# Performance work log

Hardware: AMD Instinct MI355X
Metric: run time of the kernel (lower is better)

Reference implementation:

```python
import jax, jax.numpy as jnp
import numpy as np

L = 512          # angles_max_length
R_CA = 3.8       # C-alpha - C-alpha virtual bond length (AB model)


def _B_mat(a, b):
    # Rigid transform of the AB C-alpha model: rot(alpha) about z, rot(beta), translate R along x.
    ca, sa = jnp.cos(a), jnp.sin(a)
    cb, sb = jnp.cos(b), jnp.sin(b)
    z = jnp.zeros_like(a)
    o = jnp.ones_like(a)
    rows = [
        [ca, -sa * cb,  sa * sb, R_CA * ca],
        [sa,  ca * cb, -ca * sb, R_CA * sa],
        [z,   sb,       cb,      z],
        [z,   z,        z,       o],
    ]
    return jnp.stack([jnp.stack(r, -1) for r in rows], -2)  # (..., 4, 4)


def _dB_da(a, b):
    ca, sa = jnp.cos(a), jnp.sin(a)
    cb, sb = jnp.cos(b), jnp.sin(b)
    z = jnp.zeros_like(a)
    rows = [
        [-sa, -ca * cb,  ca * sb, -R_CA * sa],
        [ ca, -sa * cb,  sa * sb,  R_CA * ca],
        [z, z, z, z],
        [z, z, z, z],
    ]
    return jnp.stack([jnp.stack(r, -1) for r in rows], -2)


def _dB_db(a, b):
    ca, sa = jnp.cos(a), jnp.sin(a)
    cb, sb = jnp.cos(b), jnp.sin(b)
    z = jnp.zeros_like(a)
    rows = [
        [z,  sa * sb,  sa * cb, z],
        [z, -ca * sb, -ca * cb, z],
        [z,  cb,      -sb,      z],
        [z, z, z, z],
    ]
    return jnp.stack([jnp.stack(r, -1) for r in rows], -2)


def setup_inputs() -> dict:
    key = jax.random.key(0)
    k1, k2, k3 = jax.random.split(key, 3)
    input_angles = jax.random.normal(k1, (32, 2, L), dtype=jnp.float32)
    input_coords = jax.random.normal(k2, (32, 3 * (L + 1)), dtype=jnp.float32)
    angles_length = jax.random.randint(k3, (32,), 0, L, dtype=jnp.int32)
    return {"input_angles": input_angles, "input_coords": input_coords,
            "angles_length": angles_length}


def reference(input_angles, input_coords, angles_length):
    Bsz = input_angles.shape[0]
    alpha = input_angles[:, 0, :]  # (B, L)
    beta = input_angles[:, 1, :]

    Bm = _B_mat(alpha, beta)  # (B, L, 4, 4)
    # Prefix products M_i = B_0 @ ... @ B_i (order-preserving associative scan).
    M = jax.lax.associative_scan(lambda x, y: x @ y, Bm, axis=1)
    eye = jnp.broadcast_to(jnp.eye(4, dtype=Bm.dtype), (Bsz, 1, 4, 4))
    M_prev = jnp.concatenate([eye, M[:, :-1]], axis=1)  # M_{i-1}

    # Rigid-transform inverse of M_i: [R^T, -R^T t; 0 1]
    Rm = M[..., :3, :3]
    t = M[..., :3, 3:]
    Rt = jnp.swapaxes(Rm, -1, -2)
    bottom = jnp.broadcast_to(jnp.array([0., 0., 0., 1.], Bm.dtype), (Bsz, L, 1, 4))
    Minv = jnp.concatenate(
        [jnp.concatenate([Rt, -(Rt @ t)], axis=-1), bottom], axis=-2)

    # F_i^q = M_{i-1} dB_i/dq M_i^{-1};  dr_j/dq_i = F_i^q r_j^h  (for j > i)
    Fa = M_prev @ _dB_da(alpha, beta) @ Minv  # (B, L, 4, 4)
    Fb = M_prev @ _dB_db(alpha, beta) @ Minv

    coords = input_coords.reshape(Bsz, L + 1, 3)
    rh = jnp.concatenate([coords, jnp.ones((Bsz, L + 1, 1), coords.dtype)], -1)

    ga = jnp.einsum('blij,bmj->blmi', Fa, rh)[..., :3]  # (B, L, L+1, 3)
    gb = jnp.einsum('blij,bmj->blmi', Fb, rh)[..., :3]

    i = jnp.arange(L)[:, None]
    j = jnp.arange(L + 1)[None, :]
    lens = angles_length[:, None, None]
    mask = ((j > i) & (i < lens) & (j <= lens))[..., None]
    ga = jnp.where(mask, ga, 0.0)
    gb = jnp.where(mask, gb, 0.0)

    out = jnp.stack([ga, gb], axis=1)  # (B, 2, L, L+1, 3)
    return out.reshape(Bsz, 2, 3 * L * (L + 1))
```

## Files before the change

### kernel.cpp

```cpp
#include <hip/hip_runtime.h>

#define LSEQ 512
#define RCA 3.8f

struct Aff { float m[3][4]; };

__device__ __forceinline__ Aff compose(const Aff& A, const Aff& B) {
    Aff C;
#pragma unroll
    for (int i = 0; i < 3; ++i) {
#pragma unroll
        for (int j = 0; j < 4; ++j) {
            float v = A.m[i][0] * B.m[0][j] + A.m[i][1] * B.m[1][j] + A.m[i][2] * B.m[2][j];
            if (j == 3) v += A.m[i][3];
            C.m[i][j] = v;
        }
    }
    return C;
}

__device__ __forceinline__ Aff shflUp(const Aff& a, int d) {
    Aff r;
#pragma unroll
    for (int i = 0; i < 3; ++i)
#pragma unroll
        for (int j = 0; j < 4; ++j)
            r.m[i][j] = __shfl_up(a.m[i][j], d, 64);
    return r;
}

__device__ __forceinline__ Aff makeB(float ca, float sa, float cb, float sb) {
    Aff B;
    B.m[0][0] = ca;  B.m[0][1] = -sa * cb; B.m[0][2] =  sa * sb; B.m[0][3] = RCA * ca;
    B.m[1][0] = sa;  B.m[1][1] =  ca * cb; B.m[1][2] = -ca * sb; B.m[1][3] = RCA * sa;
    B.m[2][0] = 0.f; B.m[2][1] =  sb;      B.m[2][2] =  cb;      B.m[2][3] = 0.f;
    return B;
}

__global__ __launch_bounds__(512) void scan_kernel(const float* __restrict__ angles,
                                                   float* __restrict__ F) {
    const int b = blockIdx.x;
    const int tid = threadIdx.x;
    const int lane = tid & 63;
    const int w = tid >> 6;

    __shared__ float sT[8][12];

    const float a  = angles[(size_t)b * 1024 + tid];
    const float be = angles[(size_t)b * 1024 + 512 + tid];
    float sa, ca, sb, cb;
    __sincosf(a, &sa, &ca);
    __sincosf(be, &sb, &cb);

    Aff S = makeB(ca, sa, cb, sb);
#pragma unroll
    for (int d = 1; d < 64; d <<= 1) {
        Aff o = shflUp(S, d);
        if (lane >= d) S = compose(o, S);
    }

    if (lane == 63) {
#pragma unroll
        for (int k = 0; k < 12; ++k) sT[w][k] = S.m[k / 4][k % 4];
    }
    __syncthreads();

    Aff E;
#pragma unroll
    for (int i = 0; i < 3; ++i)
#pragma unroll
        for (int j = 0; j < 4; ++j) E.m[i][j] = (i == j) ? 1.f : 0.f;
    for (int k = 0; k < w; ++k) {
        Aff T;
#pragma unroll
        for (int q = 0; q < 12; ++q) T.m[q / 4][q % 4] = sT[k][q];
        E = compose(E, T);
    }

    const Aff Sp = shflUp(S, 1);
    const Aff M = compose(E, S);
    Aff Mprev;
    if (lane == 0) Mprev = E;
    else           Mprev = compose(E, Sp);

    float Rt[3][3], ti[3];
#pragma unroll
    for (int i = 0; i < 3; ++i)
#pragma unroll
        for (int j = 0; j < 3; ++j) Rt[i][j] = M.m[j][i];
#pragma unroll
    for (int i = 0; i < 3; ++i)
        ti[i] = -(M.m[0][i] * M.m[0][3] + M.m[1][i] * M.m[1][3] + M.m[2][i] * M.m[2][3]);

    float d0[4] = {-sa, -ca * cb,  ca * sb, -RCA * sa};
    float d1[4] = { ca, -sa * cb,  sa * sb,  RCA * ca};
    float e01 =  sa * sb, e02 =  sa * cb;
    float e11 = -ca * sb, e12 = -ca * cb;
    float e21 =  cb,      e22 = -sb;

    float Ga[3][4], Gb[3][4];
#pragma unroll
    for (int i = 0; i < 3; ++i) {
        float p0 = Mprev.m[i][0], p1 = Mprev.m[i][1], p2 = Mprev.m[i][2];
#pragma unroll
        for (int j = 0; j < 4; ++j) Ga[i][j] = p0 * d0[j] + p1 * d1[j];
        Gb[i][0] = 0.f;
        Gb[i][1] = p0 * e01 + p1 * e11 + p2 * e21;
        Gb[i][2] = p0 * e02 + p1 * e12 + p2 * e22;
        Gb[i][3] = 0.f;
    }

    float W[24];
#pragma unroll
    for (int i = 0; i < 3; ++i) {
#pragma unroll
        for (int j = 0; j < 3; ++j) {
            W[i * 4 + j]      = Ga[i][0] * Rt[0][j] + Ga[i][1] * Rt[1][j] + Ga[i][2] * Rt[2][j];
            W[12 + i * 4 + j] = Gb[i][0] * Rt[0][j] + Gb[i][1] * Rt[1][j] + Gb[i][2] * Rt[2][j];
        }
        W[i * 4 + 3]      = Ga[i][0] * ti[0] + Ga[i][1] * ti[1] + Ga[i][2] * ti[2] + Ga[i][3];
        W[12 + i * 4 + 3] = Gb[i][0] * ti[0] + Gb[i][1] * ti[1] + Gb[i][2] * ti[2] + Gb[i][3];
    }

    float4* w4 = reinterpret_cast<float4*>(F + ((size_t)b * LSEQ + tid) * 24);
    const float4* s4 = reinterpret_cast<const float4*>(W);
#pragma unroll
    for (int q = 0; q < 6; ++q) w4[q] = s4[q];
}

__device__ __forceinline__ void st3_nt(float* p, float x, float y, float z) {
    __builtin_nontemporal_store(x, p);
    __builtin_nontemporal_store(y, p + 1);
    __builtin_nontemporal_store(z, p + 2);
}

__global__ __launch_bounds__(256) void emit_kernel(const float* __restrict__ F,
                                                   const float* __restrict__ coords,
                                                   const int* __restrict__ lens,
                                                   float* __restrict__ out) {
    const int b = blockIdx.y;
    const int l0 = blockIdx.x * 8;
    const int tid = threadIdx.x;

    __shared__ float sF[192];
    if (tid < 192) sF[tid] = F[((size_t)b * LSEQ + l0) * 24 + tid];
    __syncthreads();

    const int len = lens[b];
    const float* cp = coords + (size_t)b * 1539;

    const int m0 = tid, m1 = tid + 256, m2 = tid + 512;
    const float cx0 = cp[m0 * 3], cy0 = cp[m0 * 3 + 1], cz0 = cp[m0 * 3 + 2];
    const float cx1 = cp[m1 * 3], cy1 = cp[m1 * 3 + 1], cz1 = cp[m1 * 3 + 2];
    const bool has2 = (m2 < 513);
    float cx2 = 0.f, cy2 = 0.f, cz2 = 0.f;
    if (has2) { cx2 = cp[m2 * 3]; cy2 = cp[m2 * 3 + 1]; cz2 = cp[m2 * 3 + 2]; }

#pragma unroll
    for (int i = 0; i < 8; ++i) {
        const int l = l0 + i;
        const float* f = sF + i * 24;
        const float f00 = f[0],  f01 = f[1],  f02 = f[2],  f03 = f[3];
        const float f10 = f[4],  f11 = f[5],  f12 = f[6],  f13 = f[7];
        const float f20 = f[8],  f21 = f[9],  f22 = f[10], f23 = f[11];
        const float g00 = f[12], g01 = f[13], g02 = f[14], g03 = f[15];
        const float g10 = f[16], g11 = f[17], g12 = f[18], g13 = f[19];
        const float g20 = f[20], g21 = f[21], g22 = f[22], g23 = f[23];

        const size_t baseA = ((size_t)(b * 2) * LSEQ + l) * 1539;
        const size_t baseB = baseA + (size_t)LSEQ * 1539;
        const bool rowActive = (l < len);

        auto emit1 = [&](int m, float x, float y, float z) {
            const float s = (rowActive && (m > l) && (m <= len)) ? 1.f : 0.f;
            st3_nt(out + baseA + (size_t)m * 3,
                   s * (f00 * x + f01 * y + f02 * z + f03),
                   s * (f10 * x + f11 * y + f12 * z + f13),
                   s * (f20 * x + f21 * y + f22 * z + f23));
            st3_nt(out + baseB + (size_t)m * 3,
                   s * (g00 * x + g01 * y + g02 * z + g03),
                   s * (g10 * x + g11 * y + g12 * z + g13),
                   s * (g20 * x + g21 * y + g22 * z + g23));
        };

        emit1(m0, cx0, cy0, cz0);
        emit1(m1, cx1, cy1, cz1);
        if (has2) emit1(m2, cx2, cy2, cz2);
    }
}

extern "C" void kernel_launch(void* const* d_in, const int* in_sizes, int n_in,
                              void* d_out, int out_size, void* d_ws, size_t ws_size,
                              hipStream_t stream) {
    const float* angles = (const float*)d_in[0];
    const float* coords = (const float*)d_in[1];
    const int*   lens   = (const int*)d_in[2];
    float* out = (float*)d_out;
    float* F = (float*)d_ws;

    scan_kernel<<<32, 512, 0, stream>>>(angles, F);
    emit_kernel<<<dim3(64, 32), 256, 0, stream>>>(F, coords, lens, out);
}
```

Before: 235.6 us.

## Flatten emit kernel so each thread writes one contiguous float4 of output

Replaces the row-tiled emit kernel, which issued scalar strided nontemporal stores, with a flat kernel in which each thread computes four consecutive output floats and writes them as one aligned float4. Output indices are decoded into channel, angle, atom and component with integer divides, and coordinates and F rows are read straight from global memory and cache. This aims to fully coalesce the large output write stream, at the cost of extra index arithmetic, redundant F and coordinate loads, and dropping the nontemporal hint.

```diff
diff --git a/kernel.cpp b/kernel.cpp
--- a/kernel.cpp
+++ b/kernel.cpp
@@ -128,65 +128,46 @@
     for (int q = 0; q < 6; ++q) w4[q] = s4[q];
 }
 
-__device__ __forceinline__ void st3_nt(float* p, float x, float y, float z) {
-    __builtin_nontemporal_store(x, p);
-    __builtin_nontemporal_store(y, p + 1);
-    __builtin_nontemporal_store(z, p + 2);
-}
+__global__ __launch_bounds__(256) void emit_flat(const float* __restrict__ F,
+                                                 const float* __restrict__ coords,
+                                                 const int* __restrict__ lens,
+                                                 float* __restrict__ out) {
+    const int b = blockIdx.y;
+    const unsigned o = (blockIdx.x * 256u + threadIdx.x) * 4u;
 
-__global__ __launch_bounds__(256) void emit_kernel(const float* __restrict__ F,
-                                                   const float* __restrict__ coords,
-                                                   const int* __restrict__ lens,
-                                                   float* __restrict__ out) {
-    const int b = blockIdx.y;
-    const int l0 = blockIdx.x * 8;
-    const int tid = threadIdx.x;
+    const unsigned len = (unsigned)lens[b];
+    const float* __restrict__ Cb = coords + (size_t)b * 1539;
+    const float* __restrict__ Fb = F + (size_t)b * LSEQ * 24;
 
-    __shared__ float sF[192];
-    if (tid < 192) sF[tid] = F[((size_t)b * LSEQ + l0) * 24 + tid];
-    __syncthreads();
+    unsigned ch = (o >= 787968u) ? 1u : 0u;
+    unsigned r2 = o - ch * 787968u;
+    unsigned l  = r2 / 1539u;
+    unsigned r3 = r2 - l * 1539u;
+    unsigned m  = r3 / 3u;
+    unsigned c  = r3 - m * 3u;
 
-    const int len = lens[b];
-    const float* cp = coords + (size_t)b * 1539;
+    float v[4];
+#pragma unroll
+    for (int k = 0; k < 4; ++k) {
+        const float4 f = *reinterpret_cast<const float4*>(Fb + (l * 24u + ch * 12u + c * 4u));
+        const float x = Cb[m * 3u];
+        const float y = Cb[m * 3u + 1u];
+        const float z = Cb[m * 3u + 2u];
+        const bool act = (m > l) & (l < len) & (m <= len);
+        const float s = act ? 1.f : 0.f;
+        v[k] = s * (f.x * x + f.y * y + f.z * z + f.w);
 
-    const int m0 = tid, m1 = tid + 256, m2 = tid + 512;
-    const float cx0 = cp[m0 * 3], cy0 = cp[m0 * 3 + 1], cz0 = cp[m0 * 3 + 2];
-    const float cx1 = cp[m1 * 3], cy1 = cp[m1 * 3 + 1], cz1 = cp[m1 * 3 + 2];
-    const bool has2 = (m2 < 513);
-    float cx2 = 0.f, cy2 = 0.f, cz2 = 0.f;
-    if (has2) { cx2 = cp[m2 * 3]; cy2 = cp[m2 * 3 + 1]; cz2 = cp[m2 * 3 + 2]; }
+        if (++c == 3u) {
+            c = 0u;
+            if (++m == 513u) {
+                m = 0u;
+                if (++l == 512u) { l = 0u; ++ch; }
+            }
+        }
+    }
 
-#pragma unroll
-    for (int i = 0; i < 8; ++i) {
-        const int l = l0 + i;
-        const float* f = sF + i * 24;
-        const float f00 = f[0],  f01 = f[1],  f02 = f[2],  f03 = f[3];
-        const float f10 = f[4],  f11 = f[5],  f12 = f[6],  f13 = f[7];
-        const float f20 = f[8],  f21 = f[9],  f22 = f[10], f23 = f[11];
-        const float g00 = f[12], g01 = f[13], g02 = f[14], g03 = f[15];
-        const float g10 = f[16], g11 = f[17], g12 = f[18], g13 = f[19];
-        const float g20 = f[20], g21 = f[21], g22 = f[22], g23 = f[23];
-
-        const size_t baseA = ((size_t)(b * 2) * LSEQ + l) * 1539;
-        const size_t baseB = baseA + (size_t)LSEQ * 1539;
-        const bool rowActive = (l < len);
-
-        auto emit1 = [&](int m, float x, float y, float z) {
-            const float s = (rowActive && (m > l) && (m <= len)) ? 1.f : 0.f;
-            st3_nt(out + baseA + (size_t)m * 3,
-                   s * (f00 * x + f01 * y + f02 * z + f03),
-                   s * (f10 * x + f11 * y + f12 * z + f13),
-                   s * (f20 * x + f21 * y + f22 * z + f23));
-            st3_nt(out + baseB + (size_t)m * 3,
-                   s * (g00 * x + g01 * y + g02 * z + g03),
-                   s * (g10 * x + g11 * y + g12 * z + g13),
-                   s * (g20 * x + g21 * y + g22 * z + g23));
-        };
-
-        emit1(m0, cx0, cy0, cz0);
-        emit1(m1, cx1, cy1, cz1);
-        if (has2) emit1(m2, cx2, cy2, cz2);
-    }
+    float4 r; r.x = v[0]; r.y = v[1]; r.z = v[2]; r.w = v[3];
+    *reinterpret_cast<float4*>(out + (size_t)b * 1575936u + o) = r;
 }
 
 extern "C" void kernel_launch(void* const* d_in, const int* in_sizes, int n_in,
@@ -199,5 +180,5 @@
     float* F = (float*)d_ws;
 
     scan_kernel<<<32, 512, 0, stream>>>(angles, F);
-    emit_kernel<<<dim3(64, 32), 256, 0, stream>>>(F, coords, lens, out);
+    emit_flat<<<dim3(1539, 32), 256, 0, stream>>>(F, coords, lens, out);
 }
```

Measured after the change: 302.6 us. +28.5%, slower.

## Stage emit rows in LDS and write them out as aligned float4 stores

Applied to the files above, without the earlier changes.

The emit kernel now writes each output row's computed triples into shared-memory buffers, padded so the global row start lands on a 16-byte boundary. The row is then written to global memory with coalesced float4 stores, plus scalar head and tail stores, in place of strided 3-float nontemporal scalar stores. This targets write-coalescing inefficiency on the output, which is about 100 MB. It adds two barriers per row, serialises the row loop (unroll 1), and drops the nontemporal hint.

```diff
diff --git a/kernel.cpp b/kernel.cpp
--- a/kernel.cpp
+++ b/kernel.cpp
@@ -126,12 +126,6 @@
     const float4* s4 = reinterpret_cast<const float4*>(W);
 #pragma unroll
     for (int q = 0; q < 6; ++q) w4[q] = s4[q];
-}
-
-__device__ __forceinline__ void st3_nt(float* p, float x, float y, float z) {
-    __builtin_nontemporal_store(x, p);
-    __builtin_nontemporal_store(y, p + 1);
-    __builtin_nontemporal_store(z, p + 2);
 }
 
 __global__ __launch_bounds__(256) void emit_kernel(const float* __restrict__ F,
@@ -143,8 +137,10 @@
     const int tid = threadIdx.x;
 
     __shared__ float sF[192];
+    __shared__ float sA[1544];
+    __shared__ float sB[1544];
+
     if (tid < 192) sF[tid] = F[((size_t)b * LSEQ + l0) * 24 + tid];
-    __syncthreads();
 
     const int len = lens[b];
     const float* cp = coords + (size_t)b * 1539;
@@ -156,7 +152,9 @@
     float cx2 = 0.f, cy2 = 0.f, cz2 = 0.f;
     if (has2) { cx2 = cp[m2 * 3]; cy2 = cp[m2 * 3 + 1]; cz2 = cp[m2 * 3 + 2]; }
 
-#pragma unroll
+    __syncthreads();
+
+#pragma unroll 1
     for (int i = 0; i < 8; ++i) {
         const int l = l0 + i;
         const float* f = sF + i * 24;
@@ -167,25 +165,48 @@
         const float g10 = f[16], g11 = f[17], g12 = f[18], g13 = f[19];
         const float g20 = f[20], g21 = f[21], g22 = f[22], g23 = f[23];
 
-        const size_t baseA = ((size_t)(b * 2) * LSEQ + l) * 1539;
-        const size_t baseB = baseA + (size_t)LSEQ * 1539;
         const bool rowActive = (l < len);
-
-        auto emit1 = [&](int m, float x, float y, float z) {
+        const unsigned phase = (3u * (unsigned)l) & 3u;
+        const unsigned head  = (4u - phase) & 3u;
+        const unsigned pad   = phase;
+
+        auto cw = [&](int m, float x, float y, float z) {
             const float s = (rowActive && (m > l) && (m <= len)) ? 1.f : 0.f;
-            st3_nt(out + baseA + (size_t)m * 3,
-                   s * (f00 * x + f01 * y + f02 * z + f03),
-                   s * (f10 * x + f11 * y + f12 * z + f13),
-                   s * (f20 * x + f21 * y + f22 * z + f23));
-            st3_nt(out + baseB + (size_t)m * 3,
-                   s * (g00 * x + g01 * y + g02 * z + g03),
-                   s * (g10 * x + g11 * y + g12 * z + g13),
-                   s * (g20 * x + g21 * y + g22 * z + g23));
+            const int base = pad + m * 3;
+            sA[base + 0] = s * (f00 * x + f01 * y + f02 * z + f03);
+            sA[base + 1] = s * (f10 * x + f11 * y + f12 * z + f13);
+            sA[base + 2] = s * (f20 * x + f21 * y + f22 * z + f23);
+            sB[base + 0] = s * (g00 * x + g01 * y + g02 * z + g03);
+            sB[base + 1] = s * (g10 * x + g11 * y + g12 * z + g13);
+            sB[base + 2] = s * (g20 * x + g21 * y + g22 * z + g23);
         };
-
-        emit1(m0, cx0, cy0, cz0);
-        emit1(m1, cx1, cy1, cz1);
-        if (has2) emit1(m2, cx2, cy2, cz2);
+        cw(m0, cx0, cy0, cz0);
+        cw(m1, cx1, cy1, cz1);
+        if (has2) cw(m2, cx2, cy2, cz2);
+        __syncthreads();
+
+        const size_t rbA = ((size_t)(b * 2) * LSEQ + l) * 1539;
+        const size_t rbB = rbA + (size_t)LSEQ * 1539;
+        const unsigned n4   = (1539u - head) >> 2;
+        const unsigned tail = 1539u - head - n4 * 4u;
+
+        if (tid < (int)head) {
+            out[rbA + tid] = sA[pad + tid];
+            out[rbB + tid] = sB[pad + tid];
+        }
+        if (tid < (int)tail) {
+            const unsigned off = head + n4 * 4u + tid;
+            out[rbA + off] = sA[pad + off];
+            out[rbB + off] = sB[pad + off];
+        }
+        for (unsigned k = tid; k < n4; k += 256) {
+            const unsigned off = head + 4u * k;
+            const float4 va = *reinterpret_cast<const float4*>(sA + pad + off);
+            const float4 vb = *reinterpret_cast<const float4*>(sB + pad + off);
+            *reinterpret_cast<float4*>(out + rbA + off) = va;
+            *reinterpret_cast<float4*>(out + rbB + off) = vb;
+        }
+        __syncthreads();
     }
 }
 
```

Result: faster. 208.5 us (-11.5%).
